# Kernel optimization log

Measured on AMD Instinct MI355X. Metric: run time of the kernel, lower is better.

## Reference

```python
import jax, jax.numpy as jnp
import numpy as np

H = 8        # attention heads
G = 8        # groupnorm groups
EPS = 1e-5

def mish(x):
    return x * jnp.tanh(jnp.logaddexp(x, 0.0))

def conv1d(x, w, b, pad):
    # x: [B,C,L], w: [O,I,K]
    y = jax.lax.conv_general_dilated(x, w, (1,), [(pad, pad)],
                                     dimension_numbers=('NCH', 'OIH', 'NCH'))
    return y + b[None, :, None]

def gn_per_step(x, gamma, beta):
    # torch code reshapes [B,C,L] -> [(B L), C] and applies GroupNorm(G, C):
    # normalize each (b, l) position over channel groups.
    B, C, L = x.shape
    xg = x.reshape(B, G, C // G, L)
    mean = xg.mean(axis=2, keepdims=True)
    var = xg.var(axis=2, keepdims=True)
    xg = (xg - mean) * jax.lax.rsqrt(var + EPS)
    return xg.reshape(B, C, L) * gamma[None, :, None] + beta[None, :, None]

def layernorm(x, g, b):
    mean = x.mean(axis=-1, keepdims=True)
    var = x.var(axis=-1, keepdims=True)
    return (x - mean) * jax.lax.rsqrt(var + EPS) * g + b


def setup_inputs() -> dict:
    key = jax.random.key(0)
    ks = jax.random.split(key, 16)
    B, Cin, Cout, L, N, CD, TD = 64, 256, 512, 512, 77, 768, 512
    w = lambda k, shape, s=0.02: (jax.random.normal(k, shape, jnp.float32) * s)
    return {
        'x': jax.random.normal(ks[0], (B, Cin, L), jnp.float32),
        't': jax.random.normal(ks[1], (B, TD), jnp.float32),
        'cond': jax.random.normal(ks[2], (B, N, CD), jnp.float32),
        'conv0_w': w(ks[3], (Cout, Cin, 5)), 'conv0_b': jnp.zeros((Cout,), jnp.float32),
        'gn0_g': jnp.ones((Cout,), jnp.float32), 'gn0_b': jnp.zeros((Cout,), jnp.float32),
        'tm_w': w(ks[4], (2 * Cout, TD)), 'tm_b': jnp.zeros((2 * Cout,), jnp.float32),
        'conv1_w': w(ks[5], (Cout, Cout, 5)), 'conv1_b': jnp.zeros((Cout,), jnp.float32),
        'gn1_g': jnp.ones((Cout,), jnp.float32), 'gn1_b': jnp.zeros((Cout,), jnp.float32),
        'res_w': w(ks[6], (Cout, Cin, 1)), 'res_b': jnp.zeros((Cout,), jnp.float32),
        'ln_x_g': jnp.ones((Cout,), jnp.float32), 'ln_x_b': jnp.zeros((Cout,), jnp.float32),
        'ln_c_g': jnp.ones((CD,), jnp.float32), 'ln_c_b': jnp.zeros((CD,), jnp.float32),
        'q_w': w(ks[7], (Cout, Cout)), 'q_b': jnp.zeros((Cout,), jnp.float32),
        'k_w': w(ks[8], (Cout, CD)), 'k_b': jnp.zeros((Cout,), jnp.float32),
        'v_w': w(ks[9], (Cout, CD)), 'v_b': jnp.zeros((Cout,), jnp.float32),
        'cond_indices': jnp.arange(B, dtype=jnp.int64 if jax.config.jax_enable_x64 else jnp.int32),
    }


def _forward(x, t, cond,
             conv0_w, conv0_b, gn0_g, gn0_b, tm_w, tm_b,
             conv1_w, conv1_b, gn1_g, gn1_b, res_w, res_b,
             ln_x_g, ln_x_b, ln_c_g, ln_c_b,
             q_w, q_b, k_w, k_b, v_w, v_b, cond_indices):
    Cout = conv0_w.shape[0]
    # ---- ResidualTemporalBlock (adagn=True) ----
    ss = jnp.einsum('bi,oi->bo', mish(t), tm_w) + tm_b        # [B, 2*Cout]
    scale = ss[:, :Cout, None]                                 # chunk dim=1
    shift = ss[:, Cout:, None]
    h = conv1d(x, conv0_w, conv0_b, pad=2)                     # [B,Cout,L]
    h = gn_per_step(h, gn0_g, gn0_b)
    h = mish(h * (1.0 + scale) + shift)                        # ada_shift_scale + Mish
    h = conv1d(h, conv1_w, conv1_b, pad=2)
    h = mish(gn_per_step(h, gn1_g, gn1_b))
    out = h + conv1d(x, res_w, res_b, pad=0)                   # residual 1x1 conv
    # ---- ResidualCrossAttentionLayer (LinearCrossAttention) ----
    xs = out[cond_indices]                                     # [Bc,Cout,L]
    xi = xs.transpose(0, 2, 1)                                 # [Bc,L,Cout]
    cs = cond[cond_indices]                                    # [Bc,N,CD]
    Bc, T, D = xi.shape
    Nn = cs.shape[1]
    Dh = D // H
    q = jnp.einsum('btl,dl->btd', layernorm(xi, ln_x_g, ln_x_b), q_w) + q_b
    cn = layernorm(cs, ln_c_g, ln_c_b)
    k = jnp.einsum('bnl,dl->bnd', cn, k_w) + k_b
    v = jnp.einsum('bnl,dl->bnd', cn, v_w) + v_b
    q = jax.nn.softmax(q.reshape(Bc, T, H, Dh), axis=-1)       # softmax over head dim
    k = jax.nn.softmax(k.reshape(Bc, Nn, H, Dh), axis=1)       # softmax over tokens
    v = v.reshape(Bc, Nn, H, Dh)
    attn = jnp.einsum('bnhd,bnhl->bhdl', k, v)                 # [Bc,H,Dh,Dh] kernel
    y = jnp.einsum('bthd,bhdl->bthl', q, attn).reshape(Bc, T, D)
    return out.at[cond_indices].add(y.transpose(0, 2, 1))


def reference(x, t, cond,
              conv0_w, conv0_b, gn0_g, gn0_b, tm_w, tm_b,
              conv1_w, conv1_b, gn1_g, gn1_b, res_w, res_b,
              ln_x_g, ln_x_b, ln_c_g, ln_c_b,
              q_w, q_b, k_w, k_b, v_w, v_b, cond_indices):
    return _forward(x, t, cond, conv0_w, conv0_b, gn0_g, gn0_b, tm_w, tm_b,
                    conv1_w, conv1_b, gn1_g, gn1_b, res_w, res_b,
                    ln_x_g, ln_x_b, ln_c_g, ln_c_b,
                    q_w, q_b, k_w, k_b, v_w, v_b, cond_indices)
```

## Files before the change

### kernel.cpp

```cpp
#include <hip/hip_runtime.h>
#include <math.h>

#define EPS 1e-5f

typedef __attribute__((ext_vector_type(8))) short short8;
typedef __attribute__((ext_vector_type(4))) float floatx4;

typedef __attribute__((address_space(1))) const void* gas1_t;
typedef __attribute__((address_space(3))) void* las3_t;

__device__ __forceinline__ void glls16(const void* g, void* l) {
    __builtin_amdgcn_global_load_lds((gas1_t)g, (las3_t)l, 16, 0, 0);
}

__device__ __forceinline__ float mishf(float x) {
    float sp = fmaxf(x, 0.0f) + log1pf(expf(-fabsf(x)));
    return x * tanhf(sp);
}
__device__ __forceinline__ unsigned short f2bf(float f) {
    unsigned int u = __float_as_uint(f);
    unsigned int r = (u + 0x7fffu + ((u >> 16) & 1u)) >> 16;
    return (unsigned short)r;
}
__device__ __forceinline__ float bf2f(unsigned short s) {
    return __uint_as_float(((unsigned int)s) << 16);
}
__device__ __forceinline__ unsigned int pk2(unsigned short a, unsigned short b) {
    return (unsigned int)a | ((unsigned int)b << 16);
}

__global__ __launch_bounds__(256) void setup_k(
        const float* __restrict__ conv0_w, const float* __restrict__ conv1_w,
        const float* __restrict__ res_w, const float* __restrict__ q_w,
        const float* __restrict__ k_w, const float* __restrict__ v_w,
        const float* __restrict__ t,
        unsigned short* __restrict__ wp0, unsigned short* __restrict__ wp1,
        unsigned short* __restrict__ wr, unsigned short* __restrict__ wq,
        unsigned short* __restrict__ wk, unsigned short* __restrict__ wvv,
        float* __restrict__ mt,
        unsigned short* __restrict__ xTp, unsigned short* __restrict__ h0Tp) {
    const int blk = blockIdx.x, tid = threadIdx.x;
    if (blk < 2560) {
        int o = blk * 256 + tid;
        int ci = o & 255, co = (o >> 8) & 511, kk = o >> 17;
        wp0[o] = f2bf(conv0_w[((size_t)co * 256 + ci) * 5 + kk]);
    } else if (blk < 7680) {
        int o = (blk - 2560) * 256 + tid;
        int ci = o & 511, co = (o >> 9) & 511, kk = o >> 18;
        wp1[o] = f2bf(conv1_w[((size_t)co * 512 + ci) * 5 + kk]);
    } else if (blk < 7808) {
        int i = (blk - 7680) * 256 + tid;
        float4 f = *(const float4*)&res_w[(size_t)i * 4];
        *(uint2*)&wr[(size_t)i * 4] =
            make_uint2(pk2(f2bf(f.x), f2bf(f.y)), pk2(f2bf(f.z), f2bf(f.w)));
    } else if (blk < 8064) {
        int i = (blk - 7808) * 256 + tid;
        float4 f = *(const float4*)&q_w[(size_t)i * 4];
        *(uint2*)&wq[(size_t)i * 4] =
            make_uint2(pk2(f2bf(f.x), f2bf(f.y)), pk2(f2bf(f.z), f2bf(f.w)));
    } else if (blk < 8448) {
        int i = (blk - 8064) * 256 + tid;
        float4 f = *(const float4*)&k_w[(size_t)i * 4];
        *(uint2*)&wk[(size_t)i * 4] =
            make_uint2(pk2(f2bf(f.x), f2bf(f.y)), pk2(f2bf(f.z), f2bf(f.w)));
    } else if (blk < 8832) {
        int i = (blk - 8448) * 256 + tid;
        float4 f = *(const float4*)&v_w[(size_t)i * 4];
        *(uint2*)&wvv[(size_t)i * 4] =
            make_uint2(pk2(f2bf(f.x), f2bf(f.y)), pk2(f2bf(f.z), f2bf(f.w)));
    } else if (blk < 8960) {
        int i = (blk - 8832) * 256 + tid;
        mt[i] = mishf(t[i]);
    } else if (blk < 8992) {
        int idx = (blk - 8960) * 256 + tid;
        int u = idx * 8;
        int c = u & 255, r4 = (u >> 8) & 3, b = u >> 10;
        int row = (r4 < 2) ? r4 : (512 + r4);
        *(uint4*)&xTp[((size_t)b * 516 + row) * 256 + c] = make_uint4(0, 0, 0, 0);
    } else {
        int idx = (blk - 8992) * 256 + tid;
        int u = idx * 8;
        int c = u & 511, r4 = (u >> 9) & 3, b = u >> 11;
        int row = (r4 < 2) ? r4 : (512 + r4);
        *(uint4*)&h0Tp[((size_t)b * 516 + row) * 512 + c] = make_uint4(0, 0, 0, 0);
    }
}

__global__ __launch_bounds__(256) void xpose_cvt(const float* __restrict__ x,
        unsigned short* __restrict__ xT) {
    __shared__ float tile[64][68];
    const int tid = threadIdx.x;
    const int l0 = blockIdx.x * 64, c0 = blockIdx.y * 64, b = blockIdx.z;
    for (int idx = tid; idx < 64 * 16; idx += 256) {
        int cr = idx >> 4, lc = (idx & 15) * 4;
        float4 f = *(const float4*)&x[((size_t)b * 256 + c0 + cr) * 512 + l0 + lc];
        tile[cr][lc] = f.x; tile[cr][lc + 1] = f.y;
        tile[cr][lc + 2] = f.z; tile[cr][lc + 3] = f.w;
    }
    __syncthreads();
    for (int idx = tid; idx < 64 * 16; idx += 256) {
        int lr = idx >> 4, cc = (idx & 15) * 4;
        *(uint2*)&xT[((size_t)b * 516 + 2 + l0 + lr) * 256 + c0 + cc] =
            make_uint2(pk2(f2bf(tile[cc][lr]), f2bf(tile[cc + 1][lr])),
                       pk2(f2bf(tile[cc + 2][lr]), f2bf(tile[cc + 3][lr])));
    }
}

template<int KD>
__global__ __launch_bounds__(256) void gemm_nt(const float* __restrict__ A,
        const float* __restrict__ W, const float* __restrict__ bias,
        float* __restrict__ C, int M, int N) {
    constexpr int ST = 20;
    __shared__ __align__(16) float As[64 * ST];
    __shared__ __align__(16) float Ws[64 * ST];
    const int tid = threadIdx.x;
    const int r0 = blockIdx.x * 64, c0 = blockIdx.y * 64;
    const int tx = tid & 15, ty = tid >> 4;
    const int lrow = tid >> 2, lk = (tid & 3) * 4;
    float acc[4][4];
#pragma unroll
    for (int i = 0; i < 4; ++i)
#pragma unroll
        for (int j = 0; j < 4; ++j) acc[i][j] = 0.f;
    for (int k0 = 0; k0 < KD; k0 += 16) {
        __syncthreads();
        *(float4*)&As[lrow * ST + lk] =
            *(const float4*)&A[(size_t)(r0 + lrow) * KD + k0 + lk];
        *(float4*)&Ws[lrow * ST + lk] =
            *(const float4*)&W[(size_t)(c0 + lrow) * KD + k0 + lk];
        __syncthreads();
#pragma unroll
        for (int kk = 0; kk < 16; kk += 4) {
            float4 av[4], wv[4];
#pragma unroll
            for (int i = 0; i < 4; ++i)
                av[i] = *(const float4*)&As[(ty + 16 * i) * ST + kk];
#pragma unroll
            for (int j = 0; j < 4; ++j)
                wv[j] = *(const float4*)&Ws[(tx + 16 * j) * ST + kk];
#pragma unroll
            for (int i = 0; i < 4; ++i)
#pragma unroll
                for (int j = 0; j < 4; ++j) {
                    acc[i][j] = fmaf(av[i].x, wv[j].x, acc[i][j]);
                    acc[i][j] = fmaf(av[i].y, wv[j].y, acc[i][j]);
                    acc[i][j] = fmaf(av[i].z, wv[j].z, acc[i][j]);
                    acc[i][j] = fmaf(av[i].w, wv[j].w, acc[i][j]);
                }
        }
    }
#pragma unroll
    for (int j = 0; j < 4; ++j) {
        int c = c0 + tx + 16 * j;
        float bv = bias[c];
#pragma unroll
        for (int i = 0; i < 4; ++i)
            C[(size_t)(r0 + ty + 16 * i) * N + c] = acc[i][j] + bv;
    }
}

template<int CI, bool FILM, bool OPAD>
__global__ __launch_bounds__(256) void conv5_mfma(
        const unsigned short* __restrict__ xb,
        const unsigned short* __restrict__ wp,
        const float* __restrict__ bias,
        const float* __restrict__ gam, const float* __restrict__ bet,
        const float* __restrict__ ss,
        unsigned short* __restrict__ outT) {
    constexpr int NC = CI / 32;
    __shared__ __align__(16) unsigned short xs[2][260 * 32];
    __shared__ __align__(16) unsigned short wsm[2][5 * 64 * 32];
    __shared__ float sgam[64], sbet[64], sbias[64], sscale[64], sshift[64];

    const int tid = threadIdx.x;
    const int l0 = blockIdx.x * 256;
    const int co0 = blockIdx.y * 64;
    const int b = blockIdx.z;
    const int lane = tid & 63;
    const int wv = tid >> 6;
    const int lq = lane & 15, qd = lane >> 4;
    const int wn = wv * 64;

    if (tid < 64) {
        int co = co0 + tid;
        sbias[tid] = bias[co];
        sgam[tid] = gam[co];
        sbet[tid] = bet[co];
        if (FILM) {
            sscale[tid] = ss[(size_t)b * 1024 + co];
            sshift[tid] = ss[(size_t)b * 1024 + 512 + co];
        }
    }

    const unsigned short* gxb = xb + ((size_t)b * 516 + l0) * CI;
    const unsigned short* gwb = wp + (size_t)co0 * CI;

    const unsigned short* xsp[5];
    const unsigned short* wsp[5];
    unsigned sdo[5];
#pragma unroll
    for (int it = 0; it < 5; ++it) {
        int task = it * 256 + tid;
        {
            int ri = task >> 2, pos = task & 3;
            int seg = pos ^ ((ri >> 1) & 3);
            xsp[it] = gxb + (size_t)ri * CI + seg * 8;
        }
        {
            int kk = task >> 8, r = task & 255;
            int col = r >> 2, pos = r & 3;
            int seg = pos ^ ((col >> 1) & 3);
            wsp[it] = gwb + ((size_t)kk * 512 + col) * CI + seg * 8;
        }
        sdo[it] = (unsigned)(it * 256 + wn) * 8;
    }
    const bool xv4 = tid < 16;

    auto stage = [&](int buf) {
#pragma unroll
        for (int it = 0; it < 5; ++it) {
            if (it < 4 || xv4) glls16(xsp[it], &xs[buf][sdo[it]]);
            xsp[it] += 32;
        }
#pragma unroll
        for (int it = 0; it < 5; ++it) {
            glls16(wsp[it], &wsm[buf][sdo[it]]);
            wsp[it] += 32;
        }
    };

    unsigned bvo[5][4], avo[5][4];
#pragma unroll
    for (int kk = 0; kk < 5; ++kk) {
#pragma unroll
        for (int j = 0; j < 4; ++j) {
            int row = wn + j * 16 + lq + kk;
            int pos = qd ^ ((row >> 1) & 3);
            bvo[kk][j] = (unsigned)(row * 32 + pos * 8) * 2u;
        }
#pragma unroll
        for (int i = 0; i < 4; ++i) {
            int crow = i * 16 + lq;
            int pos = qd ^ ((crow >> 1) & 3);
            avo[kk][i] = (unsigned)(kk * 2048 + crow * 32 + pos * 8) * 2u;
        }
    }

    floatx4 acc[4][4];
#pragma unroll
    for (int i = 0; i < 4; ++i)
#pragma unroll
        for (int j = 0; j < 4; ++j) acc[i][j] = (floatx4){0.f, 0.f, 0.f, 0.f};

    auto compute = [&](int buf) {
        const char* xr = (const char*)xs[buf];
        const char* wr_ = (const char*)wsm[buf];
#pragma unroll
        for (int kk = 0; kk < 5; ++kk) {
            short8 bvf[4];
#pragma unroll
            for (int j = 0; j < 4; ++j)
                bvf[j] = *(const short8*)(xr + bvo[kk][j]);
#pragma unroll
            for (int i = 0; i < 4; ++i) {
                short8 av = *(const short8*)(wr_ + avo[kk][i]);
#pragma unroll
                for (int j = 0; j < 4; ++j)
                    acc[i][j] = __builtin_amdgcn_mfma_f32_16x16x32_bf16(
                        av, bvf[j], acc[i][j], 0, 0, 0);
            }
        }
    };

    stage(0);
    __syncthreads();
#pragma unroll 1
    for (int c = 0; c < NC; c += 2) {
        stage(1);
        compute(0);
        __syncthreads();
        if (c + 2 < NC) stage(0);
        compute(1);
        __syncthreads();
    }

    float m_[4], rs_[4];
#pragma unroll
    for (int j = 0; j < 4; ++j) {
        float s1 = 0.f, s2 = 0.f;
#pragma unroll
        for (int i = 0; i < 4; ++i) {
            float4 bv4 = *(const float4*)&sbias[i * 16 + qd * 4];
            float ba[4] = {bv4.x, bv4.y, bv4.z, bv4.w};
#pragma unroll
            for (int r = 0; r < 4; ++r) {
                float v = acc[i][j][r] + ba[r];
                acc[i][j][r] = v;
                s1 += v; s2 += v * v;
            }
        }
        s1 += __shfl_xor(s1, 16, 64); s2 += __shfl_xor(s2, 16, 64);
        s1 += __shfl_xor(s1, 32, 64); s2 += __shfl_xor(s2, 32, 64);
        float mean = s1 * (1.f / 64.f);
        float var = s2 * (1.f / 64.f) - mean * mean;
        m_[j] = mean; rs_[j] = rsqrtf(var + EPS);
    }
#pragma unroll
    for (int j = 0; j < 4; ++j) {
        int l = l0 + wn + j * 16 + lq;
        size_t rowbase = OPAD ? (((size_t)b * 516 + 2 + l) * 512 + co0)
                              : (((size_t)b * 512 + l) * 512 + co0);
#pragma unroll
        for (int i = 0; i < 4; ++i) {
            float4 g4 = *(const float4*)&sgam[i * 16 + qd * 4];
            float4 b4 = *(const float4*)&sbet[i * 16 + qd * 4];
            float ga[4] = {g4.x, g4.y, g4.z, g4.w};
            float be[4] = {b4.x, b4.y, b4.z, b4.w};
            float sa[4] = {0, 0, 0, 0}, sh[4] = {0, 0, 0, 0};
            if (FILM) {
                float4 s4 = *(const float4*)&sscale[i * 16 + qd * 4];
                float4 h4 = *(const float4*)&sshift[i * 16 + qd * 4];
                sa[0] = s4.x; sa[1] = s4.y; sa[2] = s4.z; sa[3] = s4.w;
                sh[0] = h4.x; sh[1] = h4.y; sh[2] = h4.z; sh[3] = h4.w;
            }
            unsigned short o[4];
#pragma unroll
            for (int r = 0; r < 4; ++r) {
                float v = (acc[i][j][r] - m_[j]) * rs_[j] * ga[r] + be[r];
                if (FILM) v = v * (1.f + sa[r]) + sh[r];
                o[r] = f2bf(mishf(v));
            }
            *(uint2*)&outT[rowbase + i * 16 + qd * 4] =
                make_uint2(pk2(o[0], o[1]), pk2(o[2], o[3]));
        }
    }
}

template<int KD, int EPI, bool PADA>
__global__ __launch_bounds__(256) void gemm1_mfma(
        const unsigned short* __restrict__ A,
        const unsigned short* __restrict__ W,
        const float* __restrict__ bias,
        const unsigned short* __restrict__ W2,
        const float* __restrict__ bias2,
        const unsigned short* __restrict__ addT,
        float* __restrict__ outF,
        float* __restrict__ outF2,
        unsigned short* __restrict__ outB,
        int Mreal) {
    constexpr int NC = KD / 32;
    __shared__ __align__(16) unsigned short xs[2][256 * 32];
    __shared__ __align__(16) unsigned short wsm[2][64 * 32];
    __shared__ float sbias[64];
    const int tid = threadIdx.x;
    const int m0 = blockIdx.x * 256;
    const int n0 = blockIdx.y * 64;
    const int lane = tid & 63;
    const int wv = tid >> 6;
    const int lq = lane & 15, qd = lane >> 4;
    const int wn = wv * 64;

    const unsigned short* Wu = W;
    const float* biasu = bias;
    float* outFu = outF;
    if (EPI == 2 && blockIdx.z == 1) { Wu = W2; biasu = bias2; outFu = outF2; }

    if (tid < 64) sbias[tid] = biasu[n0 + tid];

    const size_t arow0 = PADA ? ((size_t)(m0 >> 9) * 516 + 2 + (m0 & 511))
                              : (size_t)m0;
    const unsigned short* gA = A + arow0 * KD;
    const unsigned short* gW = Wu + (size_t)n0 * KD;

    const unsigned short* xp[4];
#pragma unroll
    for (int it = 0; it < 4; ++it) {
        int task = it * 256 + tid;
        int ri = task >> 2, pos = task & 3;
        int seg = pos ^ ((ri >> 1) & 3);
        xp[it] = gA + (size_t)ri * KD + seg * 8;
    }
    const unsigned short* wpq;
    {
        int col = tid >> 2, pos = tid & 3;
        int seg = pos ^ ((col >> 1) & 3);
        wpq = gW + (size_t)col * KD + seg * 8;
    }

    auto stage = [&](int buf) {
#pragma unroll
        for (int it = 0; it < 4; ++it) {
            glls16(xp[it], &xs[buf][(unsigned)(it * 256 + wn) * 8]);
            xp[it] += 32;
        }
        glls16(wpq, &wsm[buf][(unsigned)wn * 8]);
        wpq += 32;
    };

    unsigned bvo[4], avo[4];
#pragma unroll
    for (int j = 0; j < 4; ++j) {
        int row = wn + j * 16 + lq;
        int pos = qd ^ ((row >> 1) & 3);
        bvo[j] = (unsigned)(row * 32 + pos * 8) * 2u;
    }
#pragma unroll
    for (int i = 0; i < 4; ++i) {
        int crow = i * 16 + lq;
        int pos = qd ^ ((crow >> 1) & 3);
        avo[i] = (unsigned)(crow * 32 + pos * 8) * 2u;
    }

    floatx4 acc[4][4];
#pragma unroll
    for (int i = 0; i < 4; ++i)
#pragma unroll
        for (int j = 0; j < 4; ++j) acc[i][j] = (floatx4){0.f, 0.f, 0.f, 0.f};

    auto compute = [&](int buf) {
        const char* xr = (const char*)xs[buf];
        const char* wr_ = (const char*)wsm[buf];
        short8 bvf[4];
#pragma unroll
        for (int j = 0; j < 4; ++j)
            bvf[j] = *(const short8*)(xr + bvo[j]);
#pragma unroll
        for (int i = 0; i < 4; ++i) {
            short8 av = *(const short8*)(wr_ + avo[i]);
#pragma unroll
            for (int j = 0; j < 4; ++j)
                acc[i][j] = __builtin_amdgcn_mfma_f32_16x16x32_bf16(
                    av, bvf[j], acc[i][j], 0, 0, 0);
        }
    };

    stage(0);
    __syncthreads();
#pragma unroll 1
    for (int c = 0; c < NC; c += 2) {
        stage(1);
        compute(0);
        __syncthreads();
        if (c + 2 < NC) stage(0);
        compute(1);
        __syncthreads();
    }

#pragma unroll
    for (int i = 0; i < 4; ++i) {
        float4 bv4 = *(const float4*)&sbias[i * 16 + qd * 4];
        float ba[4] = {bv4.x, bv4.y, bv4.z, bv4.w};
#pragma unroll
        for (int j = 0; j < 4; ++j)
#pragma unroll
            for (int r = 0; r < 4; ++r) acc[i][j][r] += ba[r];
    }
    if (EPI == 0) {
#pragma unroll
        for (int j = 0; j < 4; ++j) {
            int m = m0 + wn + j * 16 + lq;
#pragma unroll
            for (int i = 0; i < 4; ++i) {
                int n = n0 + i * 16 + qd * 4;
                uint2 hv = *(const uint2*)&addT[(size_t)m * 512 + n];
                float vr[4];
                vr[0] = acc[i][j][0] + bf2f((unsigned short)(hv.x & 0xffff));
                vr[1] = acc[i][j][1] + bf2f((unsigned short)(hv.x >> 16));
                vr[2] = acc[i][j][2] + bf2f((unsigned short)(hv.y & 0xffff));
                vr[3] = acc[i][j][3] + bf2f((unsigned short)(hv.y >> 16));
                *(uint2*)&outB[(size_t)m * 512 + n] =
                    make_uint2(pk2(f2bf(vr[0]), f2bf(vr[1])),
                               pk2(f2bf(vr[2]), f2bf(vr[3])));
            }
        }
    } else if (EPI == 1) {
#pragma unroll
        for (int j = 0; j < 4; ++j) {
            float mx = -3.4e38f;
#pragma unroll
            for (int i = 0; i < 4; ++i)
#pragma unroll
                for (int r = 0; r < 4; ++r) mx = fmaxf(mx, acc[i][j][r]);
            mx = fmaxf(mx, __shfl_xor(mx, 16, 64));
            mx = fmaxf(mx, __shfl_xor(mx, 32, 64));
            float s = 0.f;
#pragma unroll
            for (int i = 0; i < 4; ++i)
#pragma unroll
                for (int r = 0; r < 4; ++r) {
                    float e = expf(acc[i][j][r] - mx);
                    acc[i][j][r] = e; s += e;
                }
            s += __shfl_xor(s, 16, 64);
            s += __shfl_xor(s, 32, 64);
            float inv = 1.f / s;
            int m = m0 + wn + j * 16 + lq;
#pragma unroll
            for (int i = 0; i < 4; ++i) {
                *(uint2*)&outB[(size_t)m * 512 + n0 + i * 16 + qd * 4] =
                    make_uint2(pk2(f2bf(acc[i][j][0] * inv), f2bf(acc[i][j][1] * inv)),
                               pk2(f2bf(acc[i][j][2] * inv), f2bf(acc[i][j][3] * inv)));
            }
        }
    } else {
#pragma unroll
        for (int j = 0; j < 4; ++j) {
            int m = m0 + wn + j * 16 + lq;
            if (m < Mreal) {
#pragma unroll
                for (int i = 0; i < 4; ++i) {
                    float4 o = {acc[i][j][0], acc[i][j][1], acc[i][j][2], acc[i][j][3]};
                    *(float4*)&outFu[(size_t)m * 512 + n0 + i * 16 + qd * 4] = o;
                }
            }
        }
    }
}

__global__ __launch_bounds__(256) void lnrow(const unsigned short* __restrict__ src,
        const float* __restrict__ g, const float* __restrict__ be,
        const int* __restrict__ cidx, unsigned short* __restrict__ dst) {
    const int tid = threadIdx.x;
    const int lane = tid & 63, wv = tid >> 6;
    const int row0 = blockIdx.x * 32 + wv * 8;
    for (int rr = 0; rr < 8; ++rr) {
        int m = row0 + rr;
        int b = m >> 9, t = m & 511;
        int ib = cidx[b];
        const unsigned short* sp = &src[((size_t)ib * 512 + t) * 512 + lane * 8];
        short8 u = *(const short8*)sp;
        float v[8];
        float s1 = 0.f, s2 = 0.f;
#pragma unroll
        for (int k = 0; k < 8; ++k) {
            v[k] = bf2f(((const unsigned short*)&u)[k]);
            s1 += v[k]; s2 += v[k] * v[k];
        }
#pragma unroll
        for (int o = 32; o > 0; o >>= 1) {
            s1 += __shfl_xor(s1, o, 64);
            s2 += __shfl_xor(s2, o, 64);
        }
        float mean = s1 * (1.f / 512.f);
        float var = s2 * (1.f / 512.f) - mean * mean;
        float rs = rsqrtf(var + EPS);
        float4 g0 = *(const float4*)&g[lane * 8];
        float4 g1 = *(const float4*)&g[lane * 8 + 4];
        float4 b0 = *(const float4*)&be[lane * 8];
        float4 b1 = *(const float4*)&be[lane * 8 + 4];
        float ga[8] = {g0.x, g0.y, g0.z, g0.w, g1.x, g1.y, g1.z, g1.w};
        float ba[8] = {b0.x, b0.y, b0.z, b0.w, b1.x, b1.y, b1.z, b1.w};
        unsigned short o8[8];
#pragma unroll
        for (int k = 0; k < 8; ++k)
            o8[k] = f2bf((v[k] - mean) * rs * ga[k] + ba[k]);
        *(uint4*)&dst[(size_t)m * 512 + lane * 8] =
            make_uint4(pk2(o8[0], o8[1]), pk2(o8[2], o8[3]),
                       pk2(o8[4], o8[5]), pk2(o8[6], o8[7]));
    }
}

__global__ __launch_bounds__(256) void lnc_k(const float* __restrict__ cond,
        const float* __restrict__ g, const float* __restrict__ be,
        const int* __restrict__ cidx, unsigned short* __restrict__ cn) {
    const int tid = threadIdx.x;
    const int bn = blockIdx.x;
    const int b = bn / 77, n = bn - b * 77;
    const int ib = cidx[b];
    const float* src = cond + ((size_t)ib * 77 + n) * 768;
    float v[3];
    float s = 0.f, s2 = 0.f;
#pragma unroll
    for (int i = 0; i < 3; ++i) {
        v[i] = src[tid + i * 256];
        s += v[i]; s2 += v[i] * v[i];
    }
#pragma unroll
    for (int o = 32; o > 0; o >>= 1) {
        s += __shfl_xor(s, o, 64);
        s2 += __shfl_xor(s2, o, 64);
    }
    __shared__ float r1[4], r2[4], mv[2];
    if ((tid & 63) == 0) { r1[tid >> 6] = s; r2[tid >> 6] = s2; }
    __syncthreads();
    if (tid == 0) {
        float ts = r1[0] + r1[1] + r1[2] + r1[3];
        float ts2 = r2[0] + r2[1] + r2[2] + r2[3];
        float m = ts * (1.f / 768.f);
        float var = ts2 * (1.f / 768.f) - m * m;
        mv[0] = m; mv[1] = rsqrtf(var + EPS);
    }
    __syncthreads();
    float m = mv[0], rs = mv[1];
    unsigned short* dst = cn + ((size_t)b * 77 + n) * 768;
#pragma unroll
    for (int i = 0; i < 3; ++i) {
        int c = tid + i * 256;
        dst[c] = f2bf((v[i] - m) * rs * g[c] + be[c]);
    }
}

__global__ __launch_bounds__(256) void attn_k(const float* __restrict__ k,
        const float* __restrict__ v, unsigned short* __restrict__ attnT) {
    constexpr int NS = 68;
    __shared__ __align__(16) float ks[77 * NS];
    __shared__ __align__(16) float vs[77 * NS];
    __shared__ float red[2][256];
    const int tid = threadIdx.x;
    const int b = blockIdx.x >> 3, h = blockIdx.x & 7;
    for (int idx = tid; idx < 77 * 16; idx += 256) {
        int n = idx >> 4, dq2 = (idx & 15) * 4;
        *(float4*)&ks[n * NS + dq2] =
            *(const float4*)&k[((size_t)b * 77 + n) * 512 + h * 64 + dq2];
        *(float4*)&vs[n * NS + dq2] =
            *(const float4*)&v[((size_t)b * 77 + n) * 512 + h * 64 + dq2];
    }
    __syncthreads();
    {
        const int d = tid & 63, grp = tid >> 6;
        float mx = -3.4e38f;
        for (int n = grp; n < 77; n += 4) mx = fmaxf(mx, ks[n * NS + d]);
        red[0][grp * 64 + d] = mx;
        __syncthreads();
        mx = fmaxf(fmaxf(red[0][d], red[0][64 + d]),
                   fmaxf(red[0][128 + d], red[0][192 + d]));
        float s = 0.f;
        for (int n = grp; n < 77; n += 4) {
            float e = expf(ks[n * NS + d] - mx);
            ks[n * NS + d] = e; s += e;
        }
        red[1][grp * 64 + d] = s;
        __syncthreads();
        float inv = 1.f / (red[1][d] + red[1][64 + d] + red[1][128 + d] + red[1][192 + d]);
        for (int n = grp; n < 77; n += 4) ks[n * NS + d] *= inv;
    }
    __syncthreads();
    const int e = tid & 63, dq = tid >> 6;
    float acc[16];
#pragma unroll
    for (int u = 0; u < 16; ++u) acc[u] = 0.f;
    for (int n = 0; n < 77; ++n) {
        float vv = vs[n * NS + e];
#pragma unroll
        for (int u4 = 0; u4 < 4; ++u4) {
            float4 kk = *(const float4*)&ks[n * NS + dq * 16 + u4 * 4];
            acc[u4 * 4 + 0] = fmaf(kk.x, vv, acc[u4 * 4 + 0]);
            acc[u4 * 4 + 1] = fmaf(kk.y, vv, acc[u4 * 4 + 1]);
            acc[u4 * 4 + 2] = fmaf(kk.z, vv, acc[u4 * 4 + 2]);
            acc[u4 * 4 + 3] = fmaf(kk.w, vv, acc[u4 * 4 + 3]);
        }
    }
    unsigned short ob[16];
#pragma unroll
    for (int u = 0; u < 16; ++u) ob[u] = f2bf(acc[u]);
    size_t base = (((size_t)b * 8 + h) * 64 + e) * 64 + dq * 16;
    *(uint4*)&attnT[base] = make_uint4(pk2(ob[0], ob[1]), pk2(ob[2], ob[3]),
                                       pk2(ob[4], ob[5]), pk2(ob[6], ob[7]));
    *(uint4*)&attnT[base + 8] = make_uint4(pk2(ob[8], ob[9]), pk2(ob[10], ob[11]),
                                           pk2(ob[12], ob[13]), pk2(ob[14], ob[15]));
}

__global__ __launch_bounds__(256) void yattn_final(
        const unsigned short* __restrict__ q,
        const unsigned short* __restrict__ at,
        const unsigned short* __restrict__ resT,
        const int* __restrict__ cidx, float* __restrict__ out) {
    const int tid = threadIdx.x;
    const int lane = tid & 63, wv = tid >> 6;
    const int lq = lane & 15, qd = lane >> 4;
    const int t0 = blockIdx.x * 256 + wv * 64;
    const int h = blockIdx.y, b = blockIdx.z;
    const int ib = cidx[b];
    floatx4 acc[4][4];
#pragma unroll
    for (int i = 0; i < 4; ++i)
#pragma unroll
        for (int j = 0; j < 4; ++j) acc[i][j] = (floatx4){0.f, 0.f, 0.f, 0.f};
#pragma unroll
    for (int ks = 0; ks < 2; ++ks) {
        short8 av[4], bv[4];
#pragma unroll
        for (int i = 0; i < 4; ++i)
            av[i] = *(const short8*)
                &q[((size_t)(b * 512 + t0 + i * 16 + lq)) * 512 + h * 64 + ks * 32 + qd * 8];
#pragma unroll
        for (int j = 0; j < 4; ++j)
            bv[j] = *(const short8*)
                &at[(((size_t)(b * 8 + h)) * 64 + j * 16 + lq) * 64 + ks * 32 + qd * 8];
#pragma unroll
        for (int i = 0; i < 4; ++i)
#pragma unroll
            for (int j = 0; j < 4; ++j)
                acc[i][j] = __builtin_amdgcn_mfma_f32_16x16x32_bf16(
                    av[i], bv[j], acc[i][j], 0, 0, 0);
    }
#pragma unroll
    for (int j = 0; j < 4; ++j) {
        int c = h * 64 + j * 16 + lq;
#pragma unroll
        for (int i = 0; i < 4; ++i) {
            int tb = t0 + i * 16 + qd * 4;
            float vr[4];
#pragma unroll
            for (int r = 0; r < 4; ++r)
                vr[r] = acc[i][j][r] +
                        bf2f(resT[((size_t)(ib * 512 + tb + r)) * 512 + c]);
            float4 o = {vr[0], vr[1], vr[2], vr[3]};
            *(float4*)&out[((size_t)ib * 512 + c) * 512 + tb] = o;
        }
    }
}

extern "C" void kernel_launch(void* const* d_in, const int* in_sizes, int n_in,
                              void* d_out, int out_size, void* d_ws, size_t ws_size,
                              hipStream_t stream) {
    (void)in_sizes; (void)n_in; (void)out_size; (void)ws_size;
    const float* x       = (const float*)d_in[0];
    const float* t       = (const float*)d_in[1];
    const float* cond    = (const float*)d_in[2];
    const float* conv0_w = (const float*)d_in[3];
    const float* conv0_b = (const float*)d_in[4];
    const float* gn0_g   = (const float*)d_in[5];
    const float* gn0_b   = (const float*)d_in[6];
    const float* tm_w    = (const float*)d_in[7];
    const float* tm_b    = (const float*)d_in[8];
    const float* conv1_w = (const float*)d_in[9];
    const float* conv1_b = (const float*)d_in[10];
    const float* gn1_g   = (const float*)d_in[11];
    const float* gn1_b   = (const float*)d_in[12];
    const float* res_w   = (const float*)d_in[13];
    const float* res_b   = (const float*)d_in[14];
    const float* ln_x_g  = (const float*)d_in[15];
    const float* ln_x_b  = (const float*)d_in[16];
    const float* ln_c_g  = (const float*)d_in[17];
    const float* ln_c_b  = (const float*)d_in[18];
    const float* q_w     = (const float*)d_in[19];
    const float* q_b     = (const float*)d_in[20];
    const float* k_w     = (const float*)d_in[21];
    const float* k_b     = (const float*)d_in[22];
    const float* v_w     = (const float*)d_in[23];
    const float* v_b     = (const float*)d_in[24];
    const int*   cidx    = (const int*)d_in[25];
    float* out = (float*)d_out;

    char* WS = (char*)d_ws;
    unsigned short* xTp   = (unsigned short*)(WS + 0);
    unsigned short* cnb   = (unsigned short*)(WS + 0);
    unsigned short* attnT = (unsigned short*)(WS + 8388608);
    unsigned short* h0Tp  = (unsigned short*)(WS + 16908288);
    unsigned short* xlnT  = (unsigned short*)(WS + 16908288);
    float*          kb    = (float*)(WS + 16908288);
    float*          vb    = (float*)(WS + 27000832);
    unsigned short* h1T   = (unsigned short*)(WS + 50724864);
    unsigned short* qbf   = (unsigned short*)(WS + 50724864);
    unsigned short* outTb = (unsigned short*)(WS + 84279296);
    unsigned short* wp0   = (unsigned short*)(WS + 117833728);
    unsigned short* wp1   = (unsigned short*)(WS + 119144448);
    unsigned short* wr    = (unsigned short*)(WS + 121765888);
    unsigned short* wq    = (unsigned short*)(WS + 122028032);
    unsigned short* wk    = (unsigned short*)(WS + 122552320);
    unsigned short* wvv   = (unsigned short*)(WS + 123338752);
    float*          ssb   = (float*)(WS + 124125184);
    float*          mt    = (float*)(WS + 124387328);

    setup_k<<<dim3(9056), dim3(256), 0, stream>>>(
        conv0_w, conv1_w, res_w, q_w, k_w, v_w, t,
        wp0, wp1, wr, wq, wk, wvv, mt, xTp, h0Tp);
    xpose_cvt<<<dim3(8, 4, 64), dim3(256), 0, stream>>>(x, xTp);
    gemm_nt<512><<<dim3(1, 16), dim3(256), 0, stream>>>(mt, tm_w, tm_b, ssb, 64, 1024);
    conv5_mfma<256, true, true><<<dim3(2, 8, 64), dim3(256), 0, stream>>>(
        xTp, wp0, conv0_b, gn0_g, gn0_b, ssb, h0Tp);
    conv5_mfma<512, false, false><<<dim3(2, 8, 64), dim3(256), 0, stream>>>(
        h0Tp, wp1, conv1_b, gn1_g, gn1_b, (const float*)nullptr, h1T);
    gemm1_mfma<256, 0, true><<<dim3(128, 8), dim3(256), 0, stream>>>(
        xTp, wr, res_b, (const unsigned short*)nullptr, (const float*)nullptr,
        h1T, (float*)nullptr, (float*)nullptr, outTb, 32768);
    lnrow<<<dim3(1024), dim3(256), 0, stream>>>(outTb, ln_x_g, ln_x_b, cidx, xlnT);
    gemm1_mfma<512, 1, false><<<dim3(128, 8), dim3(256), 0, stream>>>(
        xlnT, wq, q_b, (const unsigned short*)nullptr, (const float*)nullptr,
        (const unsigned short*)nullptr, (float*)nullptr, (float*)nullptr, qbf, 32768);
    lnc_k<<<dim3(4928), dim3(256), 0, stream>>>(cond, ln_c_g, ln_c_b, cidx, cnb);
    gemm1_mfma<768, 2, false><<<dim3(20, 8, 2), dim3(256), 0, stream>>>(
        cnb, wk, k_b, wvv, v_b,
        (const unsigned short*)nullptr, kb, vb, (unsigned short*)nullptr, 4928);
    attn_k<<<dim3(512), dim3(256), 0, stream>>>(kb, vb, attnT);
    yattn_final<<<dim3(2, 8, 64), dim3(256), 0, stream>>>(qbf, attnT, outTb, cidx, out);
}
```

Measured before the change: 599.8 us.

## Fuse attention kernel into output GEMM, fold cond layernorm into setup, swizzle conv blocks

Measured after the change: 983.3 us. 64.0% more time.

```diff
diff --git a/kernel.cpp b/kernel.cpp
--- a/kernel.cpp
+++ b/kernel.cpp
@@ -34,11 +34,16 @@
         const float* __restrict__ res_w, const float* __restrict__ q_w,
         const float* __restrict__ k_w, const float* __restrict__ v_w,
         const float* __restrict__ t,
+        const float* __restrict__ cond,
+        const float* __restrict__ lncg, const float* __restrict__ lncb,
+        const int* __restrict__ cidx,
         unsigned short* __restrict__ wp0, unsigned short* __restrict__ wp1,
         unsigned short* __restrict__ wr, unsigned short* __restrict__ wq,
         unsigned short* __restrict__ wk, unsigned short* __restrict__ wvv,
         float* __restrict__ mt,
-        unsigned short* __restrict__ xTp, unsigned short* __restrict__ h0Tp) {
+        unsigned short* __restrict__ xTp, unsigned short* __restrict__ h0Tp,
+        unsigned short* __restrict__ cn) {
+    __shared__ float r1[4], r2[4], mv[2];
     const int blk = blockIdx.x, tid = threadIdx.x;
     if (blk < 2560) {
         int o = blk * 256 + tid;
@@ -77,12 +82,46 @@
         int c = u & 255, r4 = (u >> 8) & 3, b = u >> 10;
         int row = (r4 < 2) ? r4 : (512 + r4);
         *(uint4*)&xTp[((size_t)b * 516 + row) * 256 + c] = make_uint4(0, 0, 0, 0);
-    } else {
+    } else if (blk < 9056) {
         int idx = (blk - 8992) * 256 + tid;
         int u = idx * 8;
         int c = u & 511, r4 = (u >> 9) & 3, b = u >> 11;
         int row = (r4 < 2) ? r4 : (512 + r4);
         *(uint4*)&h0Tp[((size_t)b * 516 + row) * 512 + c] = make_uint4(0, 0, 0, 0);
+    } else {
+        int bn = blk - 9056;
+        int b = bn / 77, n = bn - b * 77;
+        int ib = cidx[b];
+        const float* src = cond + ((size_t)ib * 77 + n) * 768;
+        float v[3];
+        float s = 0.f, s2 = 0.f;
+#pragma unroll
+        for (int i = 0; i < 3; ++i) {
+            v[i] = src[tid + i * 256];
+            s += v[i]; s2 += v[i] * v[i];
+        }
+#pragma unroll
+        for (int o = 32; o > 0; o >>= 1) {
+            s += __shfl_xor(s, o, 64);
+            s2 += __shfl_xor(s2, o, 64);
+        }
+        if ((tid & 63) == 0) { r1[tid >> 6] = s; r2[tid >> 6] = s2; }
+        __syncthreads();
+        if (tid == 0) {
+            float ts = r1[0] + r1[1] + r1[2] + r1[3];
+            float ts2 = r2[0] + r2[1] + r2[2] + r2[3];
+            float m = ts * (1.f / 768.f);
+            float var = ts2 * (1.f / 768.f) - m * m;
+            mv[0] = m; mv[1] = rsqrtf(var + EPS);
+        }
+        __syncthreads();
+        float m = mv[0], rs = mv[1];
+        unsigned short* dst = cn + ((size_t)b * 77 + n) * 768;
+#pragma unroll
+        for (int i = 0; i < 3; ++i) {
+            int c = tid + i * 256;
+            dst[c] = f2bf((v[i] - m) * rs * lncg[c] + lncb[c]);
+        }
     }
 }
 
@@ -173,9 +212,12 @@
     __shared__ float sgam[64], sbet[64], sbias[64], sscale[64], sshift[64];
 
     const int tid = threadIdx.x;
-    const int l0 = blockIdx.x * 256;
-    const int co0 = blockIdx.y * 64;
-    const int b = blockIdx.z;
+    const int id = blockIdx.x;
+    const int sN = id >> 3;
+    const int grp = ((id & 7) << 4) + (sN >> 3);
+    const int l0 = (grp & 1) * 256;
+    const int b = grp >> 1;
+    const int co0 = (sN & 7) * 64;
     const int lane = tid & 63;
     const int wv = tid >> 6;
     const int lq = lane & 15, qd = lane >> 4;
@@ -560,54 +602,21 @@
     }
 }
 
-__global__ __launch_bounds__(256) void lnc_k(const float* __restrict__ cond,
-        const float* __restrict__ g, const float* __restrict__ be,
-        const int* __restrict__ cidx, unsigned short* __restrict__ cn) {
-    const int tid = threadIdx.x;
-    const int bn = blockIdx.x;
-    const int b = bn / 77, n = bn - b * 77;
-    const int ib = cidx[b];
-    const float* src = cond + ((size_t)ib * 77 + n) * 768;
-    float v[3];
-    float s = 0.f, s2 = 0.f;
-#pragma unroll
-    for (int i = 0; i < 3; ++i) {
-        v[i] = src[tid + i * 256];
-        s += v[i]; s2 += v[i] * v[i];
-    }
-#pragma unroll
-    for (int o = 32; o > 0; o >>= 1) {
-        s += __shfl_xor(s, o, 64);
-        s2 += __shfl_xor(s2, o, 64);
-    }
-    __shared__ float r1[4], r2[4], mv[2];
-    if ((tid & 63) == 0) { r1[tid >> 6] = s; r2[tid >> 6] = s2; }
-    __syncthreads();
-    if (tid == 0) {
-        float ts = r1[0] + r1[1] + r1[2] + r1[3];
-        float ts2 = r2[0] + r2[1] + r2[2] + r2[3];
-        float m = ts * (1.f / 768.f);
-        float var = ts2 * (1.f / 768.f) - m * m;
-        mv[0] = m; mv[1] = rsqrtf(var + EPS);
-    }
-    __syncthreads();
-    float m = mv[0], rs = mv[1];
-    unsigned short* dst = cn + ((size_t)b * 77 + n) * 768;
-#pragma unroll
-    for (int i = 0; i < 3; ++i) {
-        int c = tid + i * 256;
-        dst[c] = f2bf((v[i] - m) * rs * g[c] + be[c]);
-    }
-}
-
-__global__ __launch_bounds__(256) void attn_k(const float* __restrict__ k,
-        const float* __restrict__ v, unsigned short* __restrict__ attnT) {
+__global__ __launch_bounds__(256) void yattn_fused(
+        const unsigned short* __restrict__ q,
+        const float* __restrict__ k, const float* __restrict__ v,
+        const unsigned short* __restrict__ resT,
+        const int* __restrict__ cidx, float* __restrict__ out) {
     constexpr int NS = 68;
+    constexpr int AS = 72;
     __shared__ __align__(16) float ks[77 * NS];
     __shared__ __align__(16) float vs[77 * NS];
     __shared__ float red[2][256];
+    __shared__ __align__(16) unsigned short att[64 * AS];
     const int tid = threadIdx.x;
-    const int b = blockIdx.x >> 3, h = blockIdx.x & 7;
+    const int h = blockIdx.y, b = blockIdx.z;
+    const int ib = cidx[b];
+
     for (int idx = tid; idx < 77 * 16; idx += 256) {
         int n = idx >> 4, dq2 = (idx & 15) * 4;
         *(float4*)&ks[n * NS + dq2] =
@@ -635,58 +644,51 @@
         for (int n = grp; n < 77; n += 4) ks[n * NS + d] *= inv;
     }
     __syncthreads();
-    const int e = tid & 63, dq = tid >> 6;
-    float acc[16];
-#pragma unroll
-    for (int u = 0; u < 16; ++u) acc[u] = 0.f;
-    for (int n = 0; n < 77; ++n) {
-        float vv = vs[n * NS + e];
-#pragma unroll
-        for (int u4 = 0; u4 < 4; ++u4) {
-            float4 kk = *(const float4*)&ks[n * NS + dq * 16 + u4 * 4];
-            acc[u4 * 4 + 0] = fmaf(kk.x, vv, acc[u4 * 4 + 0]);
-            acc[u4 * 4 + 1] = fmaf(kk.y, vv, acc[u4 * 4 + 1]);
-            acc[u4 * 4 + 2] = fmaf(kk.z, vv, acc[u4 * 4 + 2]);
-            acc[u4 * 4 + 3] = fmaf(kk.w, vv, acc[u4 * 4 + 3]);
-        }
-    }
-    unsigned short ob[16];
-#pragma unroll
-    for (int u = 0; u < 16; ++u) ob[u] = f2bf(acc[u]);
-    size_t base = (((size_t)b * 8 + h) * 64 + e) * 64 + dq * 16;
-    *(uint4*)&attnT[base] = make_uint4(pk2(ob[0], ob[1]), pk2(ob[2], ob[3]),
+    {
+        const int e = tid & 63, dq = tid >> 6;
+        float acc1[16];
+#pragma unroll
+        for (int u = 0; u < 16; ++u) acc1[u] = 0.f;
+        for (int n = 0; n < 77; ++n) {
+            float vv = vs[n * NS + e];
+#pragma unroll
+            for (int u4 = 0; u4 < 4; ++u4) {
+                float4 kk = *(const float4*)&ks[n * NS + dq * 16 + u4 * 4];
+                acc1[u4 * 4 + 0] = fmaf(kk.x, vv, acc1[u4 * 4 + 0]);
+                acc1[u4 * 4 + 1] = fmaf(kk.y, vv, acc1[u4 * 4 + 1]);
+                acc1[u4 * 4 + 2] = fmaf(kk.z, vv, acc1[u4 * 4 + 2]);
+                acc1[u4 * 4 + 3] = fmaf(kk.w, vv, acc1[u4 * 4 + 3]);
+            }
+        }
+        unsigned short ob[16];
+#pragma unroll
+        for (int u = 0; u < 16; ++u) ob[u] = f2bf(acc1[u]);
+        unsigned lb = (unsigned)(e * AS + dq * 16);
+        *(uint4*)&att[lb] = make_uint4(pk2(ob[0], ob[1]), pk2(ob[2], ob[3]),
                                        pk2(ob[4], ob[5]), pk2(ob[6], ob[7]));
-    *(uint4*)&attnT[base + 8] = make_uint4(pk2(ob[8], ob[9]), pk2(ob[10], ob[11]),
+        *(uint4*)&att[lb + 8] = make_uint4(pk2(ob[8], ob[9]), pk2(ob[10], ob[11]),
                                            pk2(ob[12], ob[13]), pk2(ob[14], ob[15]));
-}
-
-__global__ __launch_bounds__(256) void yattn_final(
-        const unsigned short* __restrict__ q,
-        const unsigned short* __restrict__ at,
-        const unsigned short* __restrict__ resT,
-        const int* __restrict__ cidx, float* __restrict__ out) {
-    const int tid = threadIdx.x;
+    }
+    __syncthreads();
     const int lane = tid & 63, wv = tid >> 6;
     const int lq = lane & 15, qd = lane >> 4;
     const int t0 = blockIdx.x * 256 + wv * 64;
-    const int h = blockIdx.y, b = blockIdx.z;
-    const int ib = cidx[b];
     floatx4 acc[4][4];
 #pragma unroll
     for (int i = 0; i < 4; ++i)
 #pragma unroll
         for (int j = 0; j < 4; ++j) acc[i][j] = (floatx4){0.f, 0.f, 0.f, 0.f};
 #pragma unroll
-    for (int ks = 0; ks < 2; ++ks) {
+    for (int ks2 = 0; ks2 < 2; ++ks2) {
         short8 av[4], bv[4];
 #pragma unroll
         for (int i = 0; i < 4; ++i)
             av[i] = *(const short8*)
-                &q[((size_t)(b * 512 + t0 + i * 16 + lq)) * 512 + h * 64 + ks * 32 + qd * 8];
+                &q[((size_t)(b * 512 + t0 + i * 16 + lq)) * 512 + h * 64 + ks2 * 32 + qd * 8];
 #pragma unroll
         for (int j = 0; j < 4; ++j)
             bv[j] = *(const short8*)
-                &at[(((size_t)(b * 8 + h)) * 64 + j * 16 + lq) * 64 + ks * 32 + qd * 8];
+                &att[(unsigned)((j * 16 + lq) * AS + ks2 * 32 + qd * 8)];
 #pragma unroll
         for (int i = 0; i < 4; ++i)
 #pragma unroll
@@ -745,8 +747,6 @@
 
     char* WS = (char*)d_ws;
     unsigned short* xTp   = (unsigned short*)(WS + 0);
-    unsigned short* cnb   = (unsigned short*)(WS + 0);
-    unsigned short* attnT = (unsigned short*)(WS + 8388608);
     unsigned short* h0Tp  = (unsigned short*)(WS + 16908288);
     unsigned short* xlnT  = (unsigned short*)(WS + 16908288);
     float*          kb    = (float*)(WS + 16908288);
@@ -762,15 +762,17 @@
     unsigned short* wvv   = (unsigned short*)(WS + 123338752);
     float*          ssb   = (float*)(WS + 124125184);
     float*          mt    = (float*)(WS + 124387328);
-
-    setup_k<<<dim3(9056), dim3(256), 0, stream>>>(
+    unsigned short* cnb   = (unsigned short*)(WS + 124518400);
+
+    setup_k<<<dim3(13984), dim3(256), 0, stream>>>(
         conv0_w, conv1_w, res_w, q_w, k_w, v_w, t,
-        wp0, wp1, wr, wq, wk, wvv, mt, xTp, h0Tp);
+        cond, ln_c_g, ln_c_b, cidx,
+        wp0, wp1, wr, wq, wk, wvv, mt, xTp, h0Tp, cnb);
     xpose_cvt<<<dim3(8, 4, 64), dim3(256), 0, stream>>>(x, xTp);
     gemm_nt<512><<<dim3(1, 16), dim3(256), 0, stream>>>(mt, tm_w, tm_b, ssb, 64, 1024);
-    conv5_mfma<256, true, true><<<dim3(2, 8, 64), dim3(256), 0, stream>>>(
+    conv5_mfma<256, true, true><<<dim3(1024), dim3(256), 0, stream>>>(
         xTp, wp0, conv0_b, gn0_g, gn0_b, ssb, h0Tp);
-    conv5_mfma<512, false, false><<<dim3(2, 8, 64), dim3(256), 0, stream>>>(
+    conv5_mfma<512, false, false><<<dim3(1024), dim3(256), 0, stream>>>(
         h0Tp, wp1, conv1_b, gn1_g, gn1_b, (const float*)nullptr, h1T);
     gemm1_mfma<256, 0, true><<<dim3(128, 8), dim3(256), 0, stream>>>(
         xTp, wr, res_b, (const unsigned short*)nullptr, (const float*)nullptr,
@@ -779,10 +781,9 @@
     gemm1_mfma<512, 1, false><<<dim3(128, 8), dim3(256), 0, stream>>>(
         xlnT, wq, q_b, (const unsigned short*)nullptr, (const float*)nullptr,
         (const unsigned short*)nullptr, (float*)nullptr, (float*)nullptr, qbf, 32768);
-    lnc_k<<<dim3(4928), dim3(256), 0, stream>>>(cond, ln_c_g, ln_c_b, cidx, cnb);
     gemm1_mfma<768, 2, false><<<dim3(20, 8, 2), dim3(256), 0, stream>>>(
         cnb, wk, k_b, wvv, v_b,
         (const unsigned short*)nullptr, kb, vb, (unsigned short*)nullptr, 4928);
-    attn_k<<<dim3(512), dim3(256), 0, stream>>>(kb, vb, attnT);
-    yattn_final<<<dim3(2, 8, 64), dim3(256), 0, stream>>>(qbf, attnT, outTb, cidx, out);
-}
+    yattn_fused<<<dim3(2, 8, 64), dim3(256), 0, stream>>>(
+        qbf, kb, vb, outTb, cidx, out);
+}
```
